# Kernel tuning notes

Measured on AMD Instinct MI355X. Metric: run time of the kernel, lower is better.

Reference implementation:

```python
import jax, jax.numpy as jnp
import numpy as np

HID = 300
HEADS = 4
DEPTH = 3
NA, NP_ = 50000, 15000
EA, EP, EC = 200000, 60000, 50000


def _lin(k, din, dout, scale=0.02):
    k1, k2 = jax.random.split(k)
    return (jax.random.normal(k1, (din, dout), jnp.float32) * scale,
            jax.random.normal(k2, (dout,), jnp.float32) * scale)


def _paired_edges(k, n_nodes, n_pairs):
    k1, k2 = jax.random.split(k)
    u = jax.random.randint(k1, (n_pairs,), 0, n_nodes, jnp.int32)
    v = jax.random.randint(k2, (n_pairs,), 0, n_nodes, jnp.int32)
    src = jnp.stack([u, v], 1).reshape(-1)  # edge 2k = u->v, 2k+1 = v->u
    dst = jnp.stack([v, u], 1).reshape(-1)
    return src, dst


def setup_inputs() -> dict:
    key = jax.random.key(0)
    ks = iter(jax.random.split(key, 64))
    inp = {}
    inp['f_a'] = jax.random.normal(next(ks), (NA, HID), jnp.float32)
    inp['f_p'] = jax.random.normal(next(ks), (NP_, HID), jnp.float32)
    inp['f_junc_a'] = jax.random.normal(next(ks), (NA, HID), jnp.float32)
    inp['f_junc_p'] = jax.random.normal(next(ks), (NP_, HID), jnp.float32)
    inp['x_aba'] = jax.random.normal(next(ks), (EA, HID), jnp.float32)
    inp['x_prp'] = jax.random.normal(next(ks), (EP, HID), jnp.float32)
    for tag in ('aba', 'prp'):
        for nm in ('q', 'k', 'v', 'o'):
            W, b = _lin(next(ks), HID, HID)
            inp[f'W{nm}_{tag}'] = W
            inp[f'b{nm}_{tag}'] = b
        Ws, bs = [], []
        for _ in range(DEPTH - 1):
            W, b = _lin(next(ks), HID, HID)
            Ws.append(W); bs.append(b)
        inp[f'mpW_{tag}'] = jnp.stack(Ws)
        inp[f'mpb_{tag}'] = jnp.stack(bs)
    inp['Wlast_a'], inp['blast_a'] = _lin(next(ks), 3 * HID, HID)
    inp['Wlast_p'], inp['blast_p'] = _lin(next(ks), 3 * HID, HID)
    inp['a_src'], inp['a_dst'] = _paired_edges(next(ks), NA, EA // 2)
    inp['p_src'], inp['p_dst'] = _paired_edges(next(ks), NP_, EP // 2)
    inp['ap_src'] = jax.random.randint(next(ks), (EC,), 0, NA, jnp.int32)
    inp['ap_dst'] = jax.random.randint(next(ks), (EC,), 0, NP_, jnp.int32)
    inp['pa_src'] = jax.random.randint(next(ks), (EC,), 0, NP_, jnp.int32)
    inp['pa_dst'] = jax.random.randint(next(ks), (EC,), 0, NA, jnp.int32)
    return inp


def _deg(dst, n, dtype):
    return jax.ops.segment_sum(jnp.ones(dst.shape, dtype), dst, n)


def _attn_agg(feat, edge_h, dst, n, Wq, bq, Wk, bk, Wv, bv, Wo, bo):
    """add_attn with q_len==1 == per-node segment softmax over incoming edges."""
    E = edge_h.shape[0]
    dk = HID // HEADS
    q = (feat @ Wq + bq).reshape(n, HEADS, dk)
    k = (edge_h @ Wk + bk).reshape(E, HEADS, dk)
    v = (edge_h @ Wv + bv).reshape(E, HEADS, dk)
    s = jnp.sum(q[dst] * k, -1) / jnp.sqrt(jnp.asarray(dk, feat.dtype))  # [E,H]
    smax = jax.ops.segment_max(s, dst, n)
    smax = jnp.where(jnp.isfinite(smax), smax, 0.0)
    e = jnp.exp(s - smax[dst])
    denom = jax.ops.segment_sum(e, dst, n)
    p = e / jnp.where(denom[dst] > 0, denom[dst], 1.0)
    ctx = jax.ops.segment_sum(p[..., None] * v, dst, n).reshape(n, HID)
    out = ctx @ Wo + bo
    deg = _deg(dst, n, feat.dtype)
    # nodes without incoming edges keep their feature (DGL skips them)
    return jnp.where(deg[:, None] > 0, out + feat, feat)


def _reverse_edge(h):
    E, D = h.shape
    return h.reshape(E // 2, 2, D)[:, ::-1, :].reshape(E, D)


def reference(f_a, f_p, f_junc_a, f_junc_p, x_aba, x_prp,
              Wq_aba, bq_aba, Wk_aba, bk_aba, Wv_aba, bv_aba, Wo_aba, bo_aba,
              mpW_aba, mpb_aba,
              Wq_prp, bq_prp, Wk_prp, bk_prp, Wv_prp, bv_prp, Wo_prp, bo_prp,
              mpW_prp, mpb_prp,
              Wlast_a, blast_a, Wlast_p, blast_p,
              a_src, a_dst, p_src, p_dst, ap_src, ap_dst, pa_src, pa_dst):
    fa, fp = f_a, f_p                 # f_apj fields
    fja, fjp = f_junc_a, f_junc_p     # f_junc_apj fields
    h_a, h_p = x_aba, x_prp           # edge 'h'
    for i in range(DEPTH - 1):
        # multi_update_all: attention mailbox aggregation (simultaneous)
        fa = _attn_agg(fa, h_a, a_dst, NA, Wq_aba, bq_aba, Wk_aba, bk_aba, Wv_aba, bv_aba, Wo_aba, bo_aba)
        fp = _attn_agg(fp, h_p, p_dst, NP_, Wq_prp, bq_prp, Wk_prp, bk_prp, Wv_prp, bv_prp, Wo_prp, bo_prp)
        # reverse-edge subtract + per-edge linear+ReLU
        m_a = fa[a_src] - _reverse_edge(h_a)
        h_a = jax.nn.relu(x_aba + m_a @ mpW_aba[i] + mpb_aba[i])
        m_p = fp[p_src] - _reverse_edge(h_p)
        h_p = jax.nn.relu(x_prp + m_p @ mpW_prp[i] + mpb_prp[i])
    # last homo pass: sum mailbox of edge h, concat [mail, field, f]
    mail_a = jax.ops.segment_sum(h_a, a_dst, NA)
    fa_new = jnp.concatenate([mail_a, fa, f_a], 1) @ Wlast_a + blast_a
    fa = jnp.where(_deg(a_dst, NA, fa.dtype)[:, None] > 0, fa_new, fa)
    mail_p = jax.ops.segment_sum(h_p, p_dst, NP_)
    fp_new = jnp.concatenate([mail_p, fp, f_p], 1) @ Wlast_p + blast_p
    fp = jnp.where(_deg(p_dst, NP_, fp.dtype)[:, None] > 0, fp_new, fp)
    # hetero junction pass (simultaneous: both read pre-update f_junc)
    mail_jp = jax.ops.segment_sum(fja[ap_src], ap_dst, NP_)
    fjp_new = jnp.concatenate([mail_jp, fjp, f_p], 1) @ Wlast_p + blast_p
    mail_ja = jax.ops.segment_sum(fjp[pa_src], pa_dst, NA)
    fja_new = jnp.concatenate([mail_ja, fja, f_a], 1) @ Wlast_a + blast_a
    fjp_out = jnp.where(_deg(ap_dst, NP_, fjp.dtype)[:, None] > 0, fjp_new, fjp)
    fja_out = jnp.where(_deg(pa_dst, NA, fja.dtype)[:, None] > 0, fja_new, fja)
    return jnp.concatenate([fa, fp, fja_out, fjp_out], 0)  # [2*(NA+NP_), HID]
```

## Files before the change

### kernel.cpp

```cpp
#include <hip/hip_runtime.h>

#define NA   50000
#define NP   15000
#define EA   200000
#define EP   60000
#define EC   50000
#define HID  300
#define CH   50000

#define CDIV(a,b) (((a)+(b)-1)/(b))

typedef __attribute__((ext_vector_type(8))) short short8;
typedef __attribute__((ext_vector_type(4))) float f32x4;

__device__ __forceinline__ unsigned short f2bf_rn(float f)
{
    unsigned u = __float_as_uint(f);
    unsigned r = u + 0x7fffu + ((u >> 16) & 1u);
    return (unsigned short)(r >> 16);
}

__global__ void wswz_kernel(const float* __restrict__ W,
                            unsigned short* __restrict__ Bh,
                            unsigned short* __restrict__ Bl)
{
    int t = blockIdx.x * 256 + threadIdx.x;
    if (t >= 10 * 20 * 64) return;
    int lane = t & 63;
    int f    = t >> 6;
    int nf   = f % 20;
    int s    = f / 20;
    int n    = nf * 16 + (lane & 15);
    int kb   = s * 32 + ((lane >> 4) << 3);
    short8 hv, lv;
#pragma unroll
    for (int j = 0; j < 8; ++j) {
        int k = kb + j;
        float v = (k < 300 && n < 300) ? W[k * 300 + n] : 0.f;
        unsigned u = __float_as_uint(v);
        hv[j] = (short)(u >> 16);
        float rem = v - __uint_as_float(u & 0xffff0000u);
        lv[j] = (short)f2bf_rn(rem);
    }
    *(short8*)&Bh[(size_t)t * 8] = hv;
    *(short8*)&Bl[(size_t)t * 8] = lv;
}

__global__ __launch_bounds__(256)
void gemm_mfma_kernel(const float* __restrict__ A,
                      const unsigned short* __restrict__ Bh,
                      const unsigned short* __restrict__ Bl,
                      const float* __restrict__ bias,
                      const float* __restrict__ res,
                      float* __restrict__ C,
                      int M, int accum, int relu)
{
    __shared__ unsigned short Ah[128 * 32];
    __shared__ unsigned short Al[128 * 32];
    const int tid  = threadIdx.x;
    const int lane = tid & 63;
    const int wid  = tid >> 6;
    const int wm   = wid >> 1;
    const int wn   = wid & 1;
    const int row0 = blockIdx.y * 128;
    const int nf0  = blockIdx.x * 10 + wn * 5;

    const int sr   = tid >> 1;
    const int so   = tid & 1;
    const int grow = row0 + sr;
    const bool rv  = (grow < M);
    const float* arow = A + (size_t)grow * 300;
    const int slot_base = (sr >> 4) * 64 + (sr & 15);

    f32x4 acc[4][5];
#pragma unroll
    for (int i = 0; i < 4; ++i)
#pragma unroll
        for (int j = 0; j < 5; ++j)
            acc[i][j] = (f32x4){0.f, 0.f, 0.f, 0.f};

    const float4 z4 = {0.f, 0.f, 0.f, 0.f};
    float4 ra0, ra1, ra2, ra3;

    auto load_stage = [&](int s) {
        int kb = s * 32 + so * 8;
        int kc = kb + 16;
        if (rv) {
            ra0 = (kb + 4 <= 300) ? *(const float4*)(arow + kb)     : z4;
            ra1 = (kb + 8 <= 300) ? *(const float4*)(arow + kb + 4) : z4;
            ra2 = (kc + 4 <= 300) ? *(const float4*)(arow + kc)     : z4;
            ra3 = (kc + 8 <= 300) ? *(const float4*)(arow + kc + 4) : z4;
        } else { ra0 = ra1 = ra2 = ra3 = z4; }
    };

    auto cvt_write = [&](float4 a, float4 b, int o) {
        float v[8] = {a.x, a.y, a.z, a.w, b.x, b.y, b.z, b.w};
        short8 hv, lv;
#pragma unroll
        for (int j = 0; j < 8; ++j) {
            unsigned u = __float_as_uint(v[j]);
            hv[j] = (short)(u >> 16);
            float rem = v[j] - __uint_as_float(u & 0xffff0000u);
            lv[j] = (short)f2bf_rn(rem);
        }
        int slot = slot_base + (o << 4);
        *(short8*)&Ah[slot * 8] = hv;
        *(short8*)&Al[slot * 8] = lv;
    };

    load_stage(0);
    for (int s = 0; s < 10; ++s) {
        cvt_write(ra0, ra1, so);
        cvt_write(ra2, ra3, so + 2);
        if (s < 9) load_stage(s + 1);

        const unsigned short* bp = Bh + (((size_t)s * 20 + nf0) * 64 + lane) * 8;
        const unsigned short* lp = Bl + (((size_t)s * 20 + nf0) * 64 + lane) * 8;
        short8 bh[5], bl[5];
#pragma unroll
        for (int nf = 0; nf < 5; ++nf) {
            bh[nf] = *(const short8*)(bp + nf * 512);
            bl[nf] = *(const short8*)(lp + nf * 512);
        }
        __syncthreads();

        short8 ah[4], al[4];
#pragma unroll
        for (int mf = 0; mf < 4; ++mf) {
            int slot = (wm * 4 + mf) * 64 + lane;
            ah[mf] = *(const short8*)&Ah[slot * 8];
            al[mf] = *(const short8*)&Al[slot * 8];
        }
#pragma unroll
        for (int mf = 0; mf < 4; ++mf)
#pragma unroll
            for (int nf = 0; nf < 5; ++nf) {
                acc[mf][nf] = __builtin_amdgcn_mfma_f32_16x16x32_bf16(ah[mf], bh[nf], acc[mf][nf], 0, 0, 0);
                acc[mf][nf] = __builtin_amdgcn_mfma_f32_16x16x32_bf16(ah[mf], bl[nf], acc[mf][nf], 0, 0, 0);
                acc[mf][nf] = __builtin_amdgcn_mfma_f32_16x16x32_bf16(al[mf], bh[nf], acc[mf][nf], 0, 0, 0);
            }
        __syncthreads();
    }

    const int rb = row0 + wm * 64 + (lane >> 4) * 4;
    const int cb = nf0 * 16 + (lane & 15);
#pragma unroll
    for (int mf = 0; mf < 4; ++mf) {
        int r0 = rb + mf * 16;
#pragma unroll
        for (int nf = 0; nf < 5; ++nf) {
            int col = cb + nf * 16;
            if (col >= 300) continue;
            float bv = bias ? bias[col] : 0.f;
#pragma unroll
            for (int i = 0; i < 4; ++i) {
                int row = r0 + i;
                if (row >= M) continue;
                size_t o = (size_t)row * 300 + col;
                float v = acc[mf][nf][i] + bv;
                if (res)   v += res[o];
                if (accum) v += C[o];
                if (relu)  v = fmaxf(v, 0.f);
                C[o] = v;
            }
        }
    }
}

__global__ void deg_kernel(const int* __restrict__ dst, float* __restrict__ deg, int E)
{
    int t = blockIdx.x * blockDim.x + threadIdx.x;
    if (t < E) unsafeAtomicAdd(&deg[dst[t]], 1.f);
}

__global__ void attn_score_kernel(const float* __restrict__ q, const float* __restrict__ k,
                                  const int* __restrict__ dst,
                                  float* __restrict__ es, float* __restrict__ den, int E)
{
    int t = blockIdx.x * blockDim.x + threadIdx.x;
    if (t >= E * 4) return;
    int e = t >> 2;
    int h = t & 3;
    int d = dst[e];
    const float* qp = q + (size_t)d * HID + h * 75;
    const float* kp = k + (size_t)e * HID + h * 75;
    float s = 0.f;
#pragma unroll 5
    for (int i = 0; i < 75; ++i) s = fmaf(qp[i], kp[i], s);
    float ex = expf(s * 0.11547005383792516f);
    es[t] = ex;
    unsafeAtomicAdd(&den[d * 4 + h], ex);
}

__global__ void attn_ctx_kernel(const float* __restrict__ v, const float* __restrict__ es,
                                const float* __restrict__ den, const int* __restrict__ dst,
                                float* __restrict__ ctx, int E)
{
    int t = blockIdx.x * blockDim.x + threadIdx.x;
    if (t >= E * HID) return;
    int e = t / HID;
    int dc = t - e * HID;
    int h = dc / 75;
    int d = dst[e];
    float w = es[e * 4 + h] / den[d * 4 + h];
    unsafeAtomicAdd(&ctx[(size_t)d * HID + dc], w * v[t]);
}

__global__ void masked_residual_kernel(const float* __restrict__ outp,
                                       const float* __restrict__ deg,
                                       float* __restrict__ feat, int total)
{
    int t = blockIdx.x * blockDim.x + threadIdx.x;
    if (t >= total) return;
    int n = t / HID;
    if (deg[n] > 0.f) feat[t] += outp[t];
}

__global__ void gather_sub_kernel(const float* __restrict__ feat, const float* __restrict__ h,
                                  const int* __restrict__ src, float* __restrict__ m,
                                  int mrows, int c0)
{
    int t = blockIdx.x * blockDim.x + threadIdx.x;
    if (t >= mrows * HID) return;
    int el = t / HID;
    int d  = t - el * HID;
    int ge = c0 + el;
    m[t] = feat[(size_t)src[ge] * HID + d] - h[(size_t)(ge ^ 1) * HID + d];
}

__global__ void mail_sum_kernel(const float* __restrict__ h, const int* __restrict__ dst,
                                float* __restrict__ mail, int E)
{
    int t = blockIdx.x * blockDim.x + threadIdx.x;
    if (t >= E * HID) return;
    int e = t / HID;
    int d = t - e * HID;
    unsafeAtomicAdd(&mail[(size_t)dst[e] * HID + d], h[t]);
}

__global__ void mail_gather_kernel(const float* __restrict__ feat, const int* __restrict__ src,
                                   const int* __restrict__ dst, float* __restrict__ mail, int E)
{
    int t = blockIdx.x * blockDim.x + threadIdx.x;
    if (t >= E * HID) return;
    int e = t / HID;
    int d = t - e * HID;
    unsafeAtomicAdd(&mail[(size_t)dst[e] * HID + d], feat[(size_t)src[e] * HID + d]);
}

__global__ void select_kernel(const float* __restrict__ newv, const float* __restrict__ oldv,
                              const float* __restrict__ deg, float* __restrict__ outp, int total)
{
    int t = blockIdx.x * blockDim.x + threadIdx.x;
    if (t >= total) return;
    int n = t / HID;
    outp[t] = (deg[n] > 0.f) ? newv[t] : oldv[t];
}

struct Wz { const unsigned short* h; const unsigned short* l; };

static void gemm(const float* A, Wz W, const float* bias, const float* res,
                 float* C, int M, int accum, int relu, hipStream_t s)
{
    dim3 grid(2, CDIV(M, 128));
    gemm_mfma_kernel<<<grid, 256, 0, s>>>(A, W.h, W.l, bias, res, C, M, accum, relu);
}

static void run_attn(float* feat, const float* h, const int* dst, int n, int E,
                     Wz q, const float* bq, Wz k, const float* bk,
                     Wz v, const float* bv, Wz o, const float* bo,
                     const float* deg,
                     float* Q, float* KV, float* CTX, float* ES, float* DEN,
                     hipStream_t stream)
{
    gemm(feat, q, bq, nullptr, Q, n, 0, 0, stream);
    hipMemsetAsync(DEN, 0, (size_t)n * 4 * sizeof(float), stream);
    for (int c0 = 0; c0 < E; c0 += CH) {
        int m = (E - c0 < CH) ? (E - c0) : CH;
        gemm(h + (size_t)c0 * HID, k, bk, nullptr, KV, m, 0, 0, stream);
        attn_score_kernel<<<CDIV(m * 4, 256), 256, 0, stream>>>(
            Q, KV, dst + c0, ES + (size_t)c0 * 4, DEN, m);
    }
    hipMemsetAsync(CTX, 0, (size_t)n * HID * sizeof(float), stream);
    for (int c0 = 0; c0 < E; c0 += CH) {
        int m = (E - c0 < CH) ? (E - c0) : CH;
        gemm(h + (size_t)c0 * HID, v, bv, nullptr, KV, m, 0, 0, stream);
        attn_ctx_kernel<<<CDIV(m * HID, 256), 256, 0, stream>>>(
            KV, ES + (size_t)c0 * 4, DEN, dst + c0, CTX, m);
    }
    gemm(CTX, o, bo, nullptr, Q, n, 0, 0, stream);
    masked_residual_kernel<<<CDIV(n * HID, 256), 256, 0, stream>>>(Q, deg, feat, n * HID);
}

static void run_mp(const float* feat, float* h, const float* x, const int* src,
                   Wz W, const float* b, int E, float* MB, hipStream_t stream)
{
    for (int c0 = 0; c0 < E; c0 += CH) {
        int m = (E - c0 < CH) ? (E - c0) : CH;
        gather_sub_kernel<<<CDIV(m * HID, 256), 256, 0, stream>>>(feat, h, src, MB, m, c0);
        gemm(MB, W, b, x + (size_t)c0 * HID, h + (size_t)c0 * HID, m, 0, 1, stream);
    }
}

static void last_pass(const float* mail, const float* mid, const float* first,
                      Wz w0, Wz w1, Wz w2, const float* b, const float* deg,
                      const float* oldv, float* tmp, float* outp, int n, hipStream_t stream)
{
    gemm(mail,  w0, b,       nullptr, tmp, n, 0, 0, stream);
    gemm(mid,   w1, nullptr, nullptr, tmp, n, 1, 0, stream);
    gemm(first, w2, nullptr, nullptr, tmp, n, 1, 0, stream);
    select_kernel<<<CDIV(n * HID, 256), 256, 0, stream>>>(tmp, oldv, deg, outp, n * HID);
}

extern "C" void kernel_launch(void* const* d_in, const int* in_sizes, int n_in,
                              void* d_out, int out_size, void* d_ws, size_t ws_size,
                              hipStream_t stream)
{
    (void)in_sizes; (void)n_in; (void)out_size; (void)ws_size;

    const float* f_a      = (const float*)d_in[0];
    const float* f_p      = (const float*)d_in[1];
    const float* f_junc_a = (const float*)d_in[2];
    const float* f_junc_p = (const float*)d_in[3];
    const float* x_aba    = (const float*)d_in[4];
    const float* x_prp    = (const float*)d_in[5];
    const float* Wq_aba = (const float*)d_in[6];  const float* bq_aba = (const float*)d_in[7];
    const float* Wk_aba = (const float*)d_in[8];  const float* bk_aba = (const float*)d_in[9];
    const float* Wv_aba = (const float*)d_in[10]; const float* bv_aba = (const float*)d_in[11];
    const float* Wo_aba = (const float*)d_in[12]; const float* bo_aba = (const float*)d_in[13];
    const float* mpW_aba = (const float*)d_in[14]; const float* mpb_aba = (const float*)d_in[15];
    const float* Wq_prp = (const float*)d_in[16]; const float* bq_prp = (const float*)d_in[17];
    const float* Wk_prp = (const float*)d_in[18]; const float* bk_prp = (const float*)d_in[19];
    const float* Wv_prp = (const float*)d_in[20]; const float* bv_prp = (const float*)d_in[21];
    const float* Wo_prp = (const float*)d_in[22]; const float* bo_prp = (const float*)d_in[23];
    const float* mpW_prp = (const float*)d_in[24]; const float* mpb_prp = (const float*)d_in[25];
    const float* Wlast_a = (const float*)d_in[26]; const float* blast_a = (const float*)d_in[27];
    const float* Wlast_p = (const float*)d_in[28]; const float* blast_p = (const float*)d_in[29];
    const int* a_src  = (const int*)d_in[30]; const int* a_dst  = (const int*)d_in[31];
    const int* p_src  = (const int*)d_in[32]; const int* p_dst  = (const int*)d_in[33];
    const int* ap_src = (const int*)d_in[34]; const int* ap_dst = (const int*)d_in[35];
    const int* pa_src = (const int*)d_in[36]; const int* pa_dst = (const int*)d_in[37];

    float* out = (float*)d_out;

    float* ws = (float*)d_ws;
    size_t off = 0;
    auto alloc = [&](size_t nf) {
        float* p = ws + off;
        off += (nf + 255) & ~(size_t)255;
        return p;
    };
    float* FA   = alloc((size_t)NA * HID);
    float* FP   = alloc((size_t)NP * HID);
    float* HA   = alloc((size_t)EA * HID);
    float* HP   = alloc((size_t)EP * HID);
    float* Q    = alloc((size_t)NA * HID);
    float* KV   = alloc((size_t)CH * HID);
    float* CTX  = alloc((size_t)NA * HID);
    float* ES   = alloc((size_t)EA * 4);
    float* DEN  = alloc((size_t)NA * 4);
    float* DEGA = alloc(NA);
    float* DEGP = alloc(NP);
    float* DEGPA= alloc(NA);
    float* DEGAP= alloc(NP);
    unsigned short* SWH = (unsigned short*)alloc(18 * 102400 / 2);
    unsigned short* SWL = (unsigned short*)alloc(18 * 102400 / 2);

    const float* wsrc[18] = {
        Wq_aba, Wk_aba, Wv_aba, Wo_aba,
        Wq_prp, Wk_prp, Wv_prp, Wo_prp,
        mpW_aba, mpW_aba + 90000, mpW_prp, mpW_prp + 90000,
        Wlast_a, Wlast_a + 90000, Wlast_a + 180000,
        Wlast_p, Wlast_p + 90000, Wlast_p + 180000
    };
    for (int i = 0; i < 18; ++i)
        wswz_kernel<<<50, 256, 0, stream>>>(wsrc[i],
                                            SWH + (size_t)i * 102400,
                                            SWL + (size_t)i * 102400);
    auto wz = [&](int i) { return Wz{SWH + (size_t)i * 102400, SWL + (size_t)i * 102400}; };

    hipMemsetAsync(DEGA, 0, NA * sizeof(float), stream);
    hipMemsetAsync(DEGP, 0, NP * sizeof(float), stream);
    hipMemsetAsync(DEGPA, 0, NA * sizeof(float), stream);
    hipMemsetAsync(DEGAP, 0, NP * sizeof(float), stream);
    deg_kernel<<<CDIV(EA, 256), 256, 0, stream>>>(a_dst, DEGA, EA);
    deg_kernel<<<CDIV(EP, 256), 256, 0, stream>>>(p_dst, DEGP, EP);
    deg_kernel<<<CDIV(EC, 256), 256, 0, stream>>>(pa_dst, DEGPA, EC);
    deg_kernel<<<CDIV(EC, 256), 256, 0, stream>>>(ap_dst, DEGAP, EC);

    hipMemcpyAsync(FA, f_a,   (size_t)NA * HID * sizeof(float), hipMemcpyDeviceToDevice, stream);
    hipMemcpyAsync(FP, f_p,   (size_t)NP * HID * sizeof(float), hipMemcpyDeviceToDevice, stream);
    hipMemcpyAsync(HA, x_aba, (size_t)EA * HID * sizeof(float), hipMemcpyDeviceToDevice, stream);
    hipMemcpyAsync(HP, x_prp, (size_t)EP * HID * sizeof(float), hipMemcpyDeviceToDevice, stream);

    for (int i = 0; i < 2; ++i) {
        run_attn(FA, HA, a_dst, NA, EA,
                 wz(0), bq_aba, wz(1), bk_aba, wz(2), bv_aba, wz(3), bo_aba,
                 DEGA, Q, KV, CTX, ES, DEN, stream);
        run_attn(FP, HP, p_dst, NP, EP,
                 wz(4), bq_prp, wz(5), bk_prp, wz(6), bv_prp, wz(7), bo_prp,
                 DEGP, Q, KV, CTX, ES, DEN, stream);
        run_mp(FA, HA, x_aba, a_src, wz(8 + i), mpb_aba + i * HID, EA, KV, stream);
        run_mp(FP, HP, x_prp, p_src, wz(10 + i), mpb_prp + i * HID, EP, KV, stream);
    }

    hipMemsetAsync(CTX, 0, (size_t)NA * HID * sizeof(float), stream);
    mail_sum_kernel<<<CDIV(EA * HID, 256), 256, 0, stream>>>(HA, a_dst, CTX, EA);
    last_pass(CTX, FA, f_a, wz(12), wz(13), wz(14), blast_a, DEGA, FA, Q, out, NA, stream);

    hipMemsetAsync(CTX, 0, (size_t)NP * HID * sizeof(float), stream);
    mail_sum_kernel<<<CDIV(EP * HID, 256), 256, 0, stream>>>(HP, p_dst, CTX, EP);
    last_pass(CTX, FP, f_p, wz(15), wz(16), wz(17), blast_p, DEGP, FP, Q,
              out + (size_t)NA * HID, NP, stream);

    hipMemsetAsync(CTX, 0, (size_t)NP * HID * sizeof(float), stream);
    mail_gather_kernel<<<CDIV(EC * HID, 256), 256, 0, stream>>>(f_junc_a, ap_src, ap_dst, CTX, EC);
    last_pass(CTX, f_junc_p, f_p, wz(15), wz(16), wz(17), blast_p, DEGAP, f_junc_p, Q,
              out + (size_t)(2 * NA + NP) * HID, NP, stream);

    hipMemsetAsync(CTX, 0, (size_t)NA * HID * sizeof(float), stream);
    mail_gather_kernel<<<CDIV(EC * HID, 256), 256, 0, stream>>>(f_junc_p, pa_src, pa_dst, CTX, EC);
    last_pass(CTX, f_junc_a, f_a, wz(12), wz(13), wz(14), blast_a, DEGPA, f_junc_a, Q,
              out + (size_t)(NA + NP) * HID, NA, stream);
}
```

Measured before the change: 8.484 ms.

## Widen GEMM block to full N width with double-buffered LDS for A and B

The split-bf16 MFMA GEMM now uses 512-thread blocks that each cover 128 rows by all 320 padded columns, instead of two 256-thread blocks per row tile. Each A row tile is therefore loaded and converted to hi/lo bf16 only once rather than twice. The weight fragments are staged cooperatively into LDS, and both A and B are double-buffered so the next stage's loads overlap the current MFMAs, with one barrier per stage. In exchange, LDS use and register pressure rise, there are half as many blocks, and the A layout in LDS is read with a permuted index.

```diff
diff --git a/kernel.cpp b/kernel.cpp
--- a/kernel.cpp
+++ b/kernel.cpp
@@ -46,31 +46,32 @@
     *(short8*)&Bl[(size_t)t * 8] = lv;
 }
 
-__global__ __launch_bounds__(256)
+__global__ __launch_bounds__(512)
 void gemm_mfma_kernel(const float* __restrict__ A,
-                      const unsigned short* __restrict__ Bh,
-                      const unsigned short* __restrict__ Bl,
+                      const unsigned short* __restrict__ Bhg,
+                      const unsigned short* __restrict__ Blg,
                       const float* __restrict__ bias,
                       const float* __restrict__ res,
                       float* __restrict__ C,
                       int M, int accum, int relu)
 {
-    __shared__ unsigned short Ah[128 * 32];
-    __shared__ unsigned short Al[128 * 32];
-    const int tid  = threadIdx.x;
-    const int lane = tid & 63;
-    const int wid  = tid >> 6;
-    const int wm   = wid >> 1;
-    const int wn   = wid & 1;
-    const int row0 = blockIdx.y * 128;
-    const int nf0  = blockIdx.x * 10 + wn * 5;
-
-    const int sr   = tid >> 1;
-    const int so   = tid & 1;
+    __shared__ short8 AhS[2][512];
+    __shared__ short8 AlS[2][512];
+    __shared__ short8 BhS[2][1280];
+    __shared__ short8 BlS[2][1280];
+
+    const int tid = threadIdx.x;
+    const int l   = tid & 63;
+    const int w   = tid >> 6;
+    const int wm  = w >> 2;
+    const int wn  = w & 3;
+    const int row0 = blockIdx.x * 128;
+
+    const int sr = tid >> 2;
+    const int so = tid & 3;
     const int grow = row0 + sr;
-    const bool rv  = (grow < M);
+    const bool rv = (grow < M);
     const float* arow = A + (size_t)grow * 300;
-    const int slot_base = (sr >> 4) * 64 + (sr & 15);
 
     f32x4 acc[4][5];
 #pragma unroll
@@ -80,21 +81,34 @@
             acc[i][j] = (f32x4){0.f, 0.f, 0.f, 0.f};
 
     const float4 z4 = {0.f, 0.f, 0.f, 0.f};
-    float4 ra0, ra1, ra2, ra3;
-
-    auto load_stage = [&](int s) {
+    float4 ra0, ra1;
+    short8 tb[5];
+
+    auto loadA = [&](int s) {
         int kb = s * 32 + so * 8;
-        int kc = kb + 16;
-        if (rv) {
-            ra0 = (kb + 4 <= 300) ? *(const float4*)(arow + kb)     : z4;
-            ra1 = (kb + 8 <= 300) ? *(const float4*)(arow + kb + 4) : z4;
-            ra2 = (kc + 4 <= 300) ? *(const float4*)(arow + kc)     : z4;
-            ra3 = (kc + 8 <= 300) ? *(const float4*)(arow + kc + 4) : z4;
-        } else { ra0 = ra1 = ra2 = ra3 = z4; }
-    };
-
-    auto cvt_write = [&](float4 a, float4 b, int o) {
-        float v[8] = {a.x, a.y, a.z, a.w, b.x, b.y, b.z, b.w};
+        ra0 = (rv && kb + 4 <= 300) ? *(const float4*)(arow + kb)     : z4;
+        ra1 = (rv && kb + 8 <= 300) ? *(const float4*)(arow + kb + 4) : z4;
+    };
+    auto loadB = [&](int s) {
+#pragma unroll
+        for (int q = 0; q < 5; ++q) {
+            int c = w * 5 + q;
+            const unsigned short* src = (c < 20)
+                ? Bhg + (size_t)(s * 20 + c) * 512
+                : Blg + (size_t)(s * 20 + c - 20) * 512;
+            tb[q] = *(const short8*)(src + l * 8);
+        }
+    };
+    auto writeB = [&](int b) {
+#pragma unroll
+        for (int q = 0; q < 5; ++q) {
+            int c = w * 5 + q;
+            if (c < 20) BhS[b][c * 64 + l] = tb[q];
+            else        BlS[b][(c - 20) * 64 + l] = tb[q];
+        }
+    };
+    auto cvtwriteA = [&](int b) {
+        float v[8] = {ra0.x, ra0.y, ra0.z, ra0.w, ra1.x, ra1.y, ra1.z, ra1.w};
         short8 hv, lv;
 #pragma unroll
         for (int j = 0; j < 8; ++j) {
@@ -103,53 +117,50 @@
             float rem = v[j] - __uint_as_float(u & 0xffff0000u);
             lv[j] = (short)f2bf_rn(rem);
         }
-        int slot = slot_base + (o << 4);
-        *(short8*)&Ah[slot * 8] = hv;
-        *(short8*)&Al[slot * 8] = lv;
-    };
-
-    load_stage(0);
+        AhS[b][tid] = hv;
+        AlS[b][tid] = lv;
+    };
+    auto compute = [&](int b) {
+        short8 ah[4], al[4];
+#pragma unroll
+        for (int mf = 0; mf < 4; ++mf) {
+            int idx = (wm * 4 + mf) * 64 + (l & 15) * 4 + (l >> 4);
+            ah[mf] = AhS[b][idx];
+            al[mf] = AlS[b][idx];
+        }
+#pragma unroll
+        for (int nf = 0; nf < 5; ++nf) {
+            short8 bh = BhS[b][(wn * 5 + nf) * 64 + l];
+            short8 bl = BlS[b][(wn * 5 + nf) * 64 + l];
+#pragma unroll
+            for (int mf = 0; mf < 4; ++mf) {
+                acc[mf][nf] = __builtin_amdgcn_mfma_f32_16x16x32_bf16(ah[mf], bh, acc[mf][nf], 0, 0, 0);
+                acc[mf][nf] = __builtin_amdgcn_mfma_f32_16x16x32_bf16(ah[mf], bl, acc[mf][nf], 0, 0, 0);
+                acc[mf][nf] = __builtin_amdgcn_mfma_f32_16x16x32_bf16(al[mf], bh, acc[mf][nf], 0, 0, 0);
+            }
+        }
+    };
+
+    loadA(0); loadB(0);
+    cvtwriteA(0); writeB(0);
+    __syncthreads();
+
     for (int s = 0; s < 10; ++s) {
-        cvt_write(ra0, ra1, so);
-        cvt_write(ra2, ra3, so + 2);
-        if (s < 9) load_stage(s + 1);
-
-        const unsigned short* bp = Bh + (((size_t)s * 20 + nf0) * 64 + lane) * 8;
-        const unsigned short* lp = Bl + (((size_t)s * 20 + nf0) * 64 + lane) * 8;
-        short8 bh[5], bl[5];
+        int b = s & 1;
+        if (s < 9) { loadA(s + 1); loadB(s + 1); }
+        compute(b);
+        if (s < 9) { cvtwriteA(b ^ 1); writeB(b ^ 1); }
+        __syncthreads();
+    }
+
+    const int rbase = row0 + wm * 64 + (l >> 4) * 4;
+    const int cbase = wn * 80 + (l & 15);
+#pragma unroll
+    for (int mf = 0; mf < 4; ++mf) {
+        int r0 = rbase + mf * 16;
 #pragma unroll
         for (int nf = 0; nf < 5; ++nf) {
-            bh[nf] = *(const short8*)(bp + nf * 512);
-            bl[nf] = *(const short8*)(lp + nf * 512);
-        }
-        __syncthreads();
-
-        short8 ah[4], al[4];
-#pragma unroll
-        for (int mf = 0; mf < 4; ++mf) {
-            int slot = (wm * 4 + mf) * 64 + lane;
-            ah[mf] = *(const short8*)&Ah[slot * 8];
-            al[mf] = *(const short8*)&Al[slot * 8];
-        }
-#pragma unroll
-        for (int mf = 0; mf < 4; ++mf)
-#pragma unroll
-            for (int nf = 0; nf < 5; ++nf) {
-                acc[mf][nf] = __builtin_amdgcn_mfma_f32_16x16x32_bf16(ah[mf], bh[nf], acc[mf][nf], 0, 0, 0);
-                acc[mf][nf] = __builtin_amdgcn_mfma_f32_16x16x32_bf16(ah[mf], bl[nf], acc[mf][nf], 0, 0, 0);
-                acc[mf][nf] = __builtin_amdgcn_mfma_f32_16x16x32_bf16(al[mf], bh[nf], acc[mf][nf], 0, 0, 0);
-            }
-        __syncthreads();
-    }
-
-    const int rb = row0 + wm * 64 + (lane >> 4) * 4;
-    const int cb = nf0 * 16 + (lane & 15);
-#pragma unroll
-    for (int mf = 0; mf < 4; ++mf) {
-        int r0 = rb + mf * 16;
-#pragma unroll
-        for (int nf = 0; nf < 5; ++nf) {
-            int col = cb + nf * 16;
+            int col = cbase + nf * 16;
             if (col >= 300) continue;
             float bv = bias ? bias[col] : 0.f;
 #pragma unroll
@@ -262,8 +273,7 @@
 static void gemm(const float* A, Wz W, const float* bias, const float* res,
                  float* C, int M, int accum, int relu, hipStream_t s)
 {
-    dim3 grid(2, CDIV(M, 128));
-    gemm_mfma_kernel<<<grid, 256, 0, s>>>(A, W.h, W.l, bias, res, C, M, accum, relu);
+    gemm_mfma_kernel<<<dim3(CDIV(M, 128)), 512, 0, s>>>(A, W.h, W.l, bias, res, C, M, accum, relu);
 }
 
 static void run_attn(float* feat, const float* h, const int* dst, int n, int E,
```

After: 8.569 ms. No clear change (+1.0%).
